# Performance work log

Hardware: AMD Instinct MI355X
Metric: run time of the kernel (lower is better)

## Reference

```python
import jax, jax.numpy as jnp
import numpy as np

EXPERT_CAPACITY = 1024  # per-batch per-expert capacity (token_priority <= capacity)


def setup_inputs() -> dict:
    key = jax.random.key(0)
    ks = jax.random.split(key, 5)
    B, S, D, FF, E = 2, 4096, 1024, 4096, 8
    return {
        "hidden_states": jax.random.normal(ks[0], (B, S, D), dtype=jnp.float32),
        "gate_w": jax.random.normal(ks[1], (D, E), dtype=jnp.float32) * (1.0 / np.sqrt(D)),
        "w1": jax.random.normal(ks[2], (E, D, FF), dtype=jnp.float32) * (1.0 / np.sqrt(D)),
        "w2": jax.random.normal(ks[3], (E, FF, D), dtype=jnp.float32) * (1.0 / np.sqrt(FF)),
        "w3": jax.random.normal(ks[4], (E, D, FF), dtype=jnp.float32) * (1.0 / np.sqrt(D)),
    }


def reference(hidden_states, gate_w, w1, w2, w3):
    B, S, D = hidden_states.shape
    E = gate_w.shape[1]
    C = EXPERT_CAPACITY

    # ---- route (jitter_noise = 0) ----
    router_logits = jnp.einsum("bsd,de->bse", hidden_states, gate_w)  # [B,S,E]
    router_probs = jax.nn.softmax(router_logits, axis=-1)
    sel = jnp.argmax(router_probs, axis=-1)  # [B,S] top-1 expert
    onehot = jax.nn.one_hot(sel, E, dtype=jnp.int32)  # [B,S,E]
    priority = jnp.cumsum(onehot, axis=1)  # cumsum over sequence (dim=-2)
    # position of token in its chosen expert's buffer (0-based)
    pos = jnp.take_along_axis(priority, sel[..., None], axis=-1)[..., 0] - 1  # [B,S]
    keep = pos < C  # token_priority <= expert_capacity
    max_prob = jnp.max(router_probs, axis=-1, keepdims=True)  # [B,S,1]

    # ---- dispatch: scatter kept tokens into [B,E,C,D]; dropped tokens have pos>=C -> mode='drop'
    b_idx = jnp.broadcast_to(jnp.arange(B)[:, None], (B, S))
    buf = jnp.zeros((B, E, C, D), dtype=hidden_states.dtype)
    buf = buf.at[b_idx, sel, pos].set(hidden_states, mode="drop")

    # ---- per-expert gated MLP (grouped GEMM): act(x@w1) * (x@w3) @ w2 ----
    g = jax.nn.silu(jnp.einsum("becd,edf->becf", buf, w1))
    u = jnp.einsum("becd,edf->becf", buf, w3)
    expert_out = jnp.einsum("becf,efd->becd", g * u, w2)  # [B,E,C,D]

    # ---- combine: kept tokens get expert output, dropped tokens keep hidden_states ----
    pos_g = jnp.minimum(pos, C - 1)  # safe gather index for dropped tokens
    gathered = expert_out[b_idx, sel, pos_g]  # [B,S,D]
    next_states = jnp.where(keep[..., None], gathered, hidden_states)
    out = max_prob * next_states  # dropout is identity (p=0)
    return out, router_logits
```

## Files before the change

### kernel.cpp

```cpp
#include <hip/hip_runtime.h>
#include <hip/hip_bf16.h>
#include <stdint.h>

#define B_  2
#define S_  4096
#define D_  1024
#define FF_ 4096
#define E_  8
#define C_  1024

typedef unsigned short u16;
typedef unsigned int   u32;
typedef float f32x4  __attribute__((ext_vector_type(4)));
typedef short bf16x8 __attribute__((ext_vector_type(8)));
typedef u16   u16x8  __attribute__((ext_vector_type(8)));

static __device__ __forceinline__ u16 f2bf(float f) {
    union { float f; u32 u; } v; v.f = f;
    u32 u = v.u;
    u32 r = (u + 0x7FFFu + ((u >> 16) & 1u)) >> 16;
    return (u16)r;
}

static __device__ __forceinline__ void gload_lds16(const u16* g, u16* l) {
    __builtin_amdgcn_global_load_lds(
        (const __attribute__((address_space(1))) u32*)g,
        (__attribute__((address_space(3))) u32*)l, 16, 0, 0);
}

#define BAR()    asm volatile("s_barrier" ::: "memory")
#define WAITV(n) asm volatile("s_waitcnt vmcnt(" #n ")" ::: "memory")
#define WAITL0() do { asm volatile("s_waitcnt lgkmcnt(0)" ::: "memory"); \
                      __builtin_amdgcn_sched_barrier(0); } while (0)

__global__ __launch_bounds__(256) void transpose_cvt(const float* __restrict__ src,
                                                     u16* __restrict__ dst, int K, int N) {
    __shared__ u16 t[64 * 64];
    size_t mat = (size_t)blockIdx.z * K * N;
    int n0 = blockIdx.x * 64, k0 = blockIdx.y * 64;
    int l = threadIdx.x & 63, w = threadIdx.x >> 6;
#pragma unroll
    for (int p = 0; p < 2; ++p) {
        int k = p * 32 + w * 8 + ((l >> 4) << 1);
        int n = (l & 15) * 4;
        float4 v0 = *(const float4*)&src[mat + (size_t)(k0 + k) * N + n0 + n];
        float4 v1 = *(const float4*)&src[mat + (size_t)(k0 + k + 1) * N + n0 + n];
        float a0[4] = {v0.x, v0.y, v0.z, v0.w};
        float a1[4] = {v1.x, v1.y, v1.z, v1.w};
#pragma unroll
        for (int j = 0; j < 4; ++j) {
            int nn = n + j;
            u32 pk = (u32)f2bf(a0[j]) | ((u32)f2bf(a1[j]) << 16);
            int slot = (k >> 3) ^ ((nn & 7) ^ ((nn >> 3) & 7));
            *(u32*)((char*)t + nn * 128 + slot * 16 + (k & 7) * 2) = pk;
        }
    }
    __syncthreads();
#pragma unroll
    for (int p = 0; p < 2; ++p) {
        int n = p * 32 + (threadIdx.x >> 3);
        int k8 = threadIdx.x & 7;
        int slot = k8 ^ ((n & 7) ^ ((n >> 3) & 7));
        u16x8 v = *(u16x8*)((char*)t + n * 128 + slot * 16);
        *(u16x8*)&dst[mat + (size_t)(n0 + n) * K + k0 + k8 * 8] = v;
    }
}

__global__ __launch_bounds__(256) void router_kernel(const float* __restrict__ hidden,
                                                     const float* __restrict__ gate_w,
                                                     float* __restrict__ logits_out,
                                                     int* __restrict__ sel,
                                                     float* __restrict__ maxp,
                                                     u16* __restrict__ xbf) {
    __shared__ float gw[D_ * E_];
    for (int i = threadIdx.x; i < D_ * E_ / 4; i += 256)
        ((float4*)gw)[i] = ((const float4*)gate_w)[i];
    __syncthreads();

    int wave = threadIdx.x >> 6, lane = threadIdx.x & 63;
    int tok = blockIdx.x * 4 + wave;
    const float* hrow = hidden + (size_t)tok * D_;
    u16* xrow = xbf + (size_t)tok * D_;

    double acc[8] = {0, 0, 0, 0, 0, 0, 0, 0};
#pragma unroll 4
    for (int i = 0; i < D_ / 64; i++) {
        int d = i * 64 + lane;
        float h = hrow[d];
        xrow[d] = f2bf(h);
        const float4* g4 = (const float4*)(gw + d * 8);
        float4 g0 = g4[0], g1 = g4[1];
        acc[0] += (double)h * g0.x; acc[1] += (double)h * g0.y;
        acc[2] += (double)h * g0.z; acc[3] += (double)h * g0.w;
        acc[4] += (double)h * g1.x; acc[5] += (double)h * g1.y;
        acc[6] += (double)h * g1.z; acc[7] += (double)h * g1.w;
    }
#pragma unroll
    for (int off = 32; off > 0; off >>= 1)
#pragma unroll
        for (int e = 0; e < 8; e++)
            acc[e] += __shfl_xor(acc[e], off);

    float l[8];
#pragma unroll
    for (int e = 0; e < 8; e++) l[e] = (float)acc[e];
    if (lane < 8) logits_out[(size_t)tok * 8 + lane] = l[lane];

    int am = 0; float mx = l[0];
#pragma unroll
    for (int e = 1; e < 8; e++) if (l[e] > mx) { mx = l[e]; am = e; }
    float sum = 0.f;
#pragma unroll
    for (int e = 0; e < 8; e++) sum += expf(l[e] - mx);
    if (lane == 0) { sel[tok] = am; maxp[tok] = 1.0f / sum; }
}

__global__ void scan_kernel(const int* __restrict__ sel, int* __restrict__ pos,
                            int* __restrict__ slot_token, int* __restrict__ counts) {
    int wave = threadIdx.x >> 6, lane = threadIdx.x & 63;
    int b = wave;
    int carry[8] = {0, 0, 0, 0, 0, 0, 0, 0};
    unsigned long long below = (lane == 0) ? 0ull : ((~0ull) >> (64 - lane));
    for (int s0 = 0; s0 < S_; s0 += 64) {
        int s = s0 + lane;
        int e = sel[b * S_ + s];
        int p = 0;
#pragma unroll
        for (int ex = 0; ex < 8; ex++) {
            unsigned long long m = __ballot(e == ex);
            if (e == ex) p = carry[ex] + (int)__popcll(m & below);
            carry[ex] += (int)__popcll(m);
        }
        pos[b * S_ + s] = p;
        if (p < C_) slot_token[(b * E_ + e) * C_ + p] = s;
    }
    if (lane < 8) {
        int c = carry[lane];
        counts[b * E_ + lane] = c < C_ ? c : C_;
    }
}

__global__ __launch_bounds__(512, 2) void gemm1_kernel(const u16* __restrict__ x,
                                                       const u16* __restrict__ w1t,
                                                       const u16* __restrict__ w3t,
                                                       const int* __restrict__ slot_token,
                                                       const int* __restrict__ counts,
                                                       u16* __restrict__ hbuf) {
    extern __shared__ u16 lds[];
    int phys = blockIdx.x + 32 * (blockIdx.y + 4 * blockIdx.z);
    int virt = (phys & 7) * 256 + (phys >> 3);
    int bx = virt & 31, by = (virt >> 5) & 3, bz = virt >> 7;

    int z = bz;
    int cnt = counts[z];
    int c0 = by * 256;
    if (c0 >= cnt) return;
    int n0 = bx * 128;
    int b = z >> 3, e = z & 7;

    int tid = threadIdx.x, w = tid >> 6, l = tid & 63;
    int wm = w >> 2, wn = w & 3;

    int arow0 = tid >> 2, arow1 = arow0 + 128;
    int lk = ((tid & 3) ^ ((tid >> 3) & 3)) * 8;
    int as0 = c0 + arow0, as1 = c0 + arow1;
    int tok0 = slot_token[z * C_ + (as0 < cnt ? as0 : 0)];
    int tok1 = slot_token[z * C_ + (as1 < cnt ? as1 : 0)];
    const u16* pA0 = x + ((size_t)(b * S_ + tok0)) * D_ + lk;
    const u16* pA1 = x + ((size_t)(b * S_ + tok1)) * D_ + lk;
    const u16* pB1 = w1t + ((size_t)e * FF_ + n0 + arow0) * D_ + lk;
    const u16* pB3 = w3t + ((size_t)e * FF_ + n0 + arow0) * D_ + lk;
    u32 wsl = (u32)w * 512;

    u32 ck  = (u32)(((l >> 4) ^ ((l >> 1) & 3)) * 8);
    u32 aoff  = (u32)(wm * 128 + (l & 15)) * 32 + ck;
    u32 b1off = 8192  + (u32)(wn * 32 + (l & 15)) * 32 + ck;
    u32 b3off = 12288 + (u32)(wn * 32 + (l & 15)) * 32 + ck;

    auto STAGE_A = [&](int t) {
        u16* Ls = lds + ((t & 3) << 14);
        int ko = t << 5;
        gload_lds16(pA0 + ko, Ls + wsl);
        gload_lds16(pA1 + ko, Ls + 4096 + wsl);
    };
    auto STAGE_B = [&](int t) {
        u16* Ls = lds + ((t & 3) << 14);
        int ko = t << 5;
        gload_lds16(pB1 + ko, Ls + 8192 + wsl);
        gload_lds16(pB3 + ko, Ls + 12288 + wsl);
    };

    f32x4 acc1[8][2] = {};
    f32x4 acc3[8][2] = {};

    constexpr int NK = D_ / 32;
    STAGE_A(0); STAGE_B(0); STAGE_A(1); STAGE_B(1); STAGE_A(2); STAGE_B(2);
    for (int t = 0; t < NK; ++t) {
        if (t + 2 < NK)      { WAITV(8); }
        else if (t + 1 < NK) { WAITV(4); }
        else                 { WAITV(0); }
        BAR();
        const u16* Ls = lds + ((t & 3) << 14);
        bf16x8 af[8], b1f[2], b3f[2];
#pragma unroll
        for (int f = 0; f < 4; f++) af[f] = *(const bf16x8*)(Ls + aoff + f * 512);
#pragma unroll
        for (int n = 0; n < 2; n++) {
            b1f[n] = *(const bf16x8*)(Ls + b1off + n * 512);
            b3f[n] = *(const bf16x8*)(Ls + b3off + n * 512);
        }
        if (t + 3 < NK) STAGE_A(t + 3);
        WAITL0();
        __builtin_amdgcn_s_setprio(1);
#pragma unroll
        for (int f = 0; f < 4; f++)
#pragma unroll
            for (int n = 0; n < 2; n++) {
                acc1[f][n] = __builtin_amdgcn_mfma_f32_16x16x32_bf16(af[f], b1f[n], acc1[f][n], 0, 0, 0);
                acc3[f][n] = __builtin_amdgcn_mfma_f32_16x16x32_bf16(af[f], b3f[n], acc3[f][n], 0, 0, 0);
            }
        __builtin_amdgcn_s_setprio(0);
        BAR();
#pragma unroll
        for (int f = 4; f < 8; f++) af[f] = *(const bf16x8*)(Ls + aoff + f * 512);
        if (t + 3 < NK) STAGE_B(t + 3);
        WAITL0();
        __builtin_amdgcn_s_setprio(1);
#pragma unroll
        for (int f = 4; f < 8; f++)
#pragma unroll
            for (int n = 0; n < 2; n++) {
                acc1[f][n] = __builtin_amdgcn_mfma_f32_16x16x32_bf16(af[f], b1f[n], acc1[f][n], 0, 0, 0);
                acc3[f][n] = __builtin_amdgcn_mfma_f32_16x16x32_bf16(af[f], b3f[n], acc3[f][n], 0, 0, 0);
            }
        __builtin_amdgcn_s_setprio(0);
    }

#pragma unroll
    for (int f = 0; f < 8; f++) {
        int row = wm * 128 + f * 16 + ((l >> 4) << 2);
#pragma unroll
        for (int r = 0; r < 4; r++) {
            int slot = c0 + row + r;
            if (slot < cnt) {
                size_t base = ((size_t)z * C_ + slot) * FF_ + n0 + wn * 32 + (l & 15);
#pragma unroll
                for (int n = 0; n < 2; n++) {
                    float g = acc1[f][n][r], uu = acc3[f][n][r];
                    float h = (g / (1.f + __expf(-g))) * uu;
                    hbuf[base + n * 16] = f2bf(h);
                }
            }
        }
    }
}

__global__ __launch_bounds__(512, 2) void gemm2_kernel(const u16* __restrict__ hbuf,
                                                       const u16* __restrict__ w2t,
                                                       const int* __restrict__ slot_token,
                                                       const int* __restrict__ counts,
                                                       const float* __restrict__ maxp,
                                                       float* __restrict__ out) {
    extern __shared__ u16 lds[];
    int phys = blockIdx.x + 4 * (blockIdx.y + 4 * blockIdx.z);
    int virt = (phys & 7) * 32 + (phys >> 3);
    int bx = virt & 3, by = (virt >> 2) & 3, bz = virt >> 4;

    int z = bz;
    int cnt = counts[z];
    int c0 = by * 256;
    if (c0 >= cnt) return;
    int n0 = bx * 256;
    int b = z >> 3, e = z & 7;

    int tid = threadIdx.x, w = tid >> 6, l = tid & 63;
    int wm = w >> 2, wn = w & 3;

    int arow0 = tid >> 2;
    int lk = ((tid & 3) ^ ((tid >> 3) & 3)) * 8;
    const u16* pA0 = hbuf + ((size_t)z * C_ + c0 + arow0) * FF_ + lk;
    const u16* pA1 = pA0 + (size_t)128 * FF_;
    const u16* pB0 = w2t + ((size_t)e * D_ + n0 + arow0) * FF_ + lk;
    const u16* pB1 = pB0 + (size_t)128 * FF_;
    u32 wsl = (u32)w * 512;

    u32 ck  = (u32)(((l >> 4) ^ ((l >> 1) & 3)) * 8);
    u32 aoff = (u32)(wm * 128 + (l & 15)) * 32 + ck;
    u32 boff = 8192 + (u32)(wn * 64 + (l & 15)) * 32 + ck;

    auto STAGE_A = [&](int t) {
        u16* Ls = lds + ((t & 3) << 14);
        int ko = t << 5;
        gload_lds16(pA0 + ko, Ls + wsl);
        gload_lds16(pA1 + ko, Ls + 4096 + wsl);
    };
    auto STAGE_B = [&](int t) {
        u16* Ls = lds + ((t & 3) << 14);
        int ko = t << 5;
        gload_lds16(pB0 + ko, Ls + 8192 + wsl);
        gload_lds16(pB1 + ko, Ls + 12288 + wsl);
    };

    f32x4 acc[8][4] = {};

    constexpr int NK = FF_ / 32;
    STAGE_A(0); STAGE_B(0); STAGE_A(1); STAGE_B(1); STAGE_A(2); STAGE_B(2);
    for (int t = 0; t < NK; ++t) {
        if (t + 2 < NK)      { WAITV(8); }
        else if (t + 1 < NK) { WAITV(4); }
        else                 { WAITV(0); }
        BAR();
        const u16* Ls = lds + ((t & 3) << 14);
        bf16x8 af[8], bfv[4];
#pragma unroll
        for (int f = 0; f < 4; f++) af[f] = *(const bf16x8*)(Ls + aoff + f * 512);
#pragma unroll
        for (int n = 0; n < 4; n++) bfv[n] = *(const bf16x8*)(Ls + boff + n * 512);
        if (t + 3 < NK) STAGE_A(t + 3);
        WAITL0();
        __builtin_amdgcn_s_setprio(1);
#pragma unroll
        for (int f = 0; f < 4; f++)
#pragma unroll
            for (int n = 0; n < 4; n++)
                acc[f][n] = __builtin_amdgcn_mfma_f32_16x16x32_bf16(af[f], bfv[n], acc[f][n], 0, 0, 0);
        __builtin_amdgcn_s_setprio(0);
        BAR();
#pragma unroll
        for (int f = 4; f < 8; f++) af[f] = *(const bf16x8*)(Ls + aoff + f * 512);
        if (t + 3 < NK) STAGE_B(t + 3);
        WAITL0();
        __builtin_amdgcn_s_setprio(1);
#pragma unroll
        for (int f = 4; f < 8; f++)
#pragma unroll
            for (int n = 0; n < 4; n++)
                acc[f][n] = __builtin_amdgcn_mfma_f32_16x16x32_bf16(af[f], bfv[n], acc[f][n], 0, 0, 0);
        __builtin_amdgcn_s_setprio(0);
    }

#pragma unroll
    for (int f = 0; f < 8; f++) {
        int row = wm * 128 + f * 16 + ((l >> 4) << 2);
#pragma unroll
        for (int r = 0; r < 4; r++) {
            int slot = c0 + row + r;
            if (slot < cnt) {
                int s = slot_token[z * C_ + slot];
                float sc = maxp[b * S_ + s];
                float* orow = out + ((size_t)b * S_ + s) * D_ + n0 + wn * 64 + (l & 15);
#pragma unroll
                for (int n = 0; n < 4; n++)
                    orow[n * 16] = sc * acc[f][n][r];
            }
        }
    }
}

__global__ __launch_bounds__(256) void combine_dropped(const float* __restrict__ hidden,
                                                       const int* __restrict__ pos,
                                                       const float* __restrict__ maxp,
                                                       float* __restrict__ out) {
    int t = blockIdx.x;
    if (pos[t] < C_) return;
    float sc = maxp[t];
    const float* src = hidden + (size_t)t * D_;
    float* dst = out + (size_t)t * D_;
    for (int d = threadIdx.x; d < D_; d += 256) dst[d] = sc * src[d];
}

extern "C" void kernel_launch(void* const* d_in, const int* in_sizes, int n_in,
                              void* d_out, int out_size, void* d_ws, size_t ws_size,
                              hipStream_t stream) {
    const float* hidden = (const float*)d_in[0];
    const float* gate_w = (const float*)d_in[1];
    const float* w1     = (const float*)d_in[2];
    const float* w2     = (const float*)d_in[3];
    const float* w3     = (const float*)d_in[4];

    float* out        = (float*)d_out;
    float* logits_out = out + (size_t)B_ * S_ * D_;

    char* ws = (char*)d_ws;
    u16* hidden_bf = (u16*)ws;            ws += (size_t)B_ * S_ * D_ * 2;
    u16* w1t       = (u16*)ws;            ws += (size_t)E_ * D_ * FF_ * 2;
    u16* w3t       = (u16*)ws;            ws += (size_t)E_ * D_ * FF_ * 2;
    u16* w2t       = (u16*)ws;            ws += (size_t)E_ * D_ * FF_ * 2;
    u16* hbuf      = (u16*)ws;            ws += (size_t)B_ * E_ * C_ * FF_ * 2;
    int*   sel        = (int*)ws;         ws += (size_t)B_ * S_ * 4;
    int*   pos        = (int*)ws;         ws += (size_t)B_ * S_ * 4;
    float* maxp       = (float*)ws;       ws += (size_t)B_ * S_ * 4;
    int*   slot_token = (int*)ws;         ws += (size_t)B_ * E_ * C_ * 4;
    int*   counts     = (int*)ws;         ws += (size_t)B_ * E_ * 4;

    (void)hipFuncSetAttribute((const void*)gemm1_kernel,
                              hipFuncAttributeMaxDynamicSharedMemorySize, 131072);
    (void)hipFuncSetAttribute((const void*)gemm2_kernel,
                              hipFuncAttributeMaxDynamicSharedMemorySize, 131072);

    router_kernel<<<B_ * S_ / 4, 256, 0, stream>>>(hidden, gate_w, logits_out, sel, maxp, hidden_bf);
    scan_kernel<<<1, 128, 0, stream>>>(sel, pos, slot_token, counts);

    transpose_cvt<<<dim3(FF_ / 64, D_ / 64, E_), 256, 0, stream>>>(w1, w1t, D_, FF_);
    transpose_cvt<<<dim3(FF_ / 64, D_ / 64, E_), 256, 0, stream>>>(w3, w3t, D_, FF_);
    transpose_cvt<<<dim3(D_ / 64, FF_ / 64, E_), 256, 0, stream>>>(w2, w2t, FF_, D_);

    gemm1_kernel<<<dim3(32, 4, 16), 512, 131072, stream>>>(hidden_bf, w1t, w3t, slot_token, counts, hbuf);
    gemm2_kernel<<<dim3(4, 4, 16), 512, 131072, stream>>>(hbuf, w2t, slot_token, counts, maxp, out);
    combine_dropped<<<B_ * S_, 256, 0, stream>>>(hidden, pos, maxp, out);
}
```

Baseline: 490.8 us.

## Pre-gather routed tokens into contiguous bf16 buffer and parallelize scan

```diff
diff --git a/kernel.cpp b/kernel.cpp
--- a/kernel.cpp
+++ b/kernel.cpp
@@ -70,8 +70,7 @@
                                                      const float* __restrict__ gate_w,
                                                      float* __restrict__ logits_out,
                                                      int* __restrict__ sel,
-                                                     float* __restrict__ maxp,
-                                                     u16* __restrict__ xbf) {
+                                                     float* __restrict__ maxp) {
     __shared__ float gw[D_ * E_];
     for (int i = threadIdx.x; i < D_ * E_ / 4; i += 256)
         ((float4*)gw)[i] = ((const float4*)gate_w)[i];
@@ -80,14 +79,12 @@
     int wave = threadIdx.x >> 6, lane = threadIdx.x & 63;
     int tok = blockIdx.x * 4 + wave;
     const float* hrow = hidden + (size_t)tok * D_;
-    u16* xrow = xbf + (size_t)tok * D_;
 
     double acc[8] = {0, 0, 0, 0, 0, 0, 0, 0};
 #pragma unroll 4
     for (int i = 0; i < D_ / 64; i++) {
         int d = i * 64 + lane;
         float h = hrow[d];
-        xrow[d] = f2bf(h);
         const float4* g4 = (const float4*)(gw + d * 8);
         float4 g0 = g4[0], g1 = g4[1];
         acc[0] += (double)h * g0.x; acc[1] += (double)h * g0.y;
@@ -115,15 +112,50 @@
     if (lane == 0) { sel[tok] = am; maxp[tok] = 1.0f / sum; }
 }
 
-__global__ void scan_kernel(const int* __restrict__ sel, int* __restrict__ pos,
-                            int* __restrict__ slot_token, int* __restrict__ counts) {
-    int wave = threadIdx.x >> 6, lane = threadIdx.x & 63;
-    int b = wave;
-    int carry[8] = {0, 0, 0, 0, 0, 0, 0, 0};
-    unsigned long long below = (lane == 0) ? 0ull : ((~0ull) >> (64 - lane));
-    for (int s0 = 0; s0 < S_; s0 += 64) {
-        int s = s0 + lane;
-        int e = sel[b * S_ + s];
+__global__ __launch_bounds__(1024) void scan_kernel(const int* __restrict__ sel,
+                                                    int* __restrict__ pos,
+                                                    int* __restrict__ slot_token,
+                                                    int* __restrict__ counts) {
+    __shared__ int hist[16][8];
+    __shared__ int base[16][8];
+    int b = blockIdx.x;
+    int tid = threadIdx.x, wv = tid >> 6, l = tid & 63;
+    unsigned long long below = (l == 0) ? 0ull : ((~0ull) >> (64 - l));
+    const int* sb = sel + b * S_;
+
+    int eloc[4];
+    int cnt[8] = {0, 0, 0, 0, 0, 0, 0, 0};
+#pragma unroll
+    for (int c = 0; c < 4; c++) {
+        int s = wv * 256 + c * 64 + l;
+        int e = sb[s];
+        eloc[c] = e;
+#pragma unroll
+        for (int ex = 0; ex < 8; ex++)
+            cnt[ex] += (int)__popcll(__ballot(e == ex));
+    }
+    if (l == 0)
+#pragma unroll
+        for (int ex = 0; ex < 8; ex++) hist[wv][ex] = cnt[ex];
+    __syncthreads();
+    if (tid < 128) {
+        int ex = tid & 7, v = tid >> 3;
+        int s = 0;
+        for (int w2 = 0; w2 < v; w2++) s += hist[w2][ex];
+        base[v][ex] = s;
+        if (v == 15) {
+            int tot = s + hist[15][ex];
+            counts[b * 8 + ex] = tot < C_ ? tot : C_;
+        }
+    }
+    __syncthreads();
+    int carry[8];
+#pragma unroll
+    for (int ex = 0; ex < 8; ex++) carry[ex] = base[wv][ex];
+#pragma unroll
+    for (int c = 0; c < 4; c++) {
+        int s = wv * 256 + c * 64 + l;
+        int e = eloc[c];
         int p = 0;
 #pragma unroll
         for (int ex = 0; ex < 8; ex++) {
@@ -134,16 +166,35 @@
         pos[b * S_ + s] = p;
         if (p < C_) slot_token[(b * E_ + e) * C_ + p] = s;
     }
-    if (lane < 8) {
-        int c = carry[lane];
-        counts[b * E_ + lane] = c < C_ ? c : C_;
-    }
-}
-
-__global__ __launch_bounds__(512, 2) void gemm1_kernel(const u16* __restrict__ x,
+}
+
+__global__ __launch_bounds__(256) void gather_kernel(const float* __restrict__ hidden,
+                                                     const int* __restrict__ slot_token,
+                                                     const int* __restrict__ counts,
+                                                     u16* __restrict__ xg) {
+    int z = blockIdx.x >> 8;
+    int r0 = (blockIdx.x & 255) * 4;
+    int cnt = counts[z];
+    int slot = r0 + (threadIdx.x >> 6);
+    if (slot >= cnt) return;
+    int l = threadIdx.x & 63;
+    int b = z >> 3;
+    int tok = slot_token[z * C_ + slot];
+    const float4* src = (const float4*)(hidden + (size_t)(b * S_ + tok) * D_) + l * 4;
+    u16x8* dst = (u16x8*)(xg + ((size_t)z * C_ + slot) * D_) + l * 2;
+#pragma unroll
+    for (int h = 0; h < 2; h++) {
+        float4 a = src[h * 2], c = src[h * 2 + 1];
+        u16x8 o;
+        o[0] = f2bf(a.x); o[1] = f2bf(a.y); o[2] = f2bf(a.z); o[3] = f2bf(a.w);
+        o[4] = f2bf(c.x); o[5] = f2bf(c.y); o[6] = f2bf(c.z); o[7] = f2bf(c.w);
+        dst[h] = o;
+    }
+}
+
+__global__ __launch_bounds__(512, 2) void gemm1_kernel(const u16* __restrict__ xg,
                                                        const u16* __restrict__ w1t,
                                                        const u16* __restrict__ w3t,
-                                                       const int* __restrict__ slot_token,
                                                        const int* __restrict__ counts,
                                                        u16* __restrict__ hbuf) {
     extern __shared__ u16 lds[];
@@ -156,21 +207,19 @@
     int c0 = by * 256;
     if (c0 >= cnt) return;
     int n0 = bx * 128;
-    int b = z >> 3, e = z & 7;
+    int e = z & 7;
 
     int tid = threadIdx.x, w = tid >> 6, l = tid & 63;
     int wm = w >> 2, wn = w & 3;
 
-    int arow0 = tid >> 2, arow1 = arow0 + 128;
+    int arow0 = tid >> 2;
     int lk = ((tid & 3) ^ ((tid >> 3) & 3)) * 8;
-    int as0 = c0 + arow0, as1 = c0 + arow1;
-    int tok0 = slot_token[z * C_ + (as0 < cnt ? as0 : 0)];
-    int tok1 = slot_token[z * C_ + (as1 < cnt ? as1 : 0)];
-    const u16* pA0 = x + ((size_t)(b * S_ + tok0)) * D_ + lk;
-    const u16* pA1 = x + ((size_t)(b * S_ + tok1)) * D_ + lk;
+    const u16* pA0 = xg + ((size_t)z * C_ + c0 + arow0) * D_ + lk;
+    const u16* pA1 = pA0 + (size_t)128 * D_;
     const u16* pB1 = w1t + ((size_t)e * FF_ + n0 + arow0) * D_ + lk;
     const u16* pB3 = w3t + ((size_t)e * FF_ + n0 + arow0) * D_ + lk;
-    u32 wsl = (u32)w * 512;
+    u32 wA0 = (u32)tid * 8, wA1 = (u32)tid * 8 + 4096;
+    u32 wB1 = 8192 + (u32)tid * 8, wB3 = 12288 + (u32)tid * 8;
 
     u32 ck  = (u32)(((l >> 4) ^ ((l >> 1) & 3)) * 8);
     u32 aoff  = (u32)(wm * 128 + (l & 15)) * 32 + ck;
@@ -180,14 +229,14 @@
     auto STAGE_A = [&](int t) {
         u16* Ls = lds + ((t & 3) << 14);
         int ko = t << 5;
-        gload_lds16(pA0 + ko, Ls + wsl);
-        gload_lds16(pA1 + ko, Ls + 4096 + wsl);
+        gload_lds16(pA0 + ko, Ls + wA0);
+        gload_lds16(pA1 + ko, Ls + wA1);
     };
     auto STAGE_B = [&](int t) {
         u16* Ls = lds + ((t & 3) << 14);
         int ko = t << 5;
-        gload_lds16(pB1 + ko, Ls + 8192 + wsl);
-        gload_lds16(pB3 + ko, Ls + 12288 + wsl);
+        gload_lds16(pB1 + ko, Ls + wB1);
+        gload_lds16(pB3 + ko, Ls + wB3);
     };
 
     f32x4 acc1[8][2] = {};
@@ -240,13 +289,13 @@
     for (int f = 0; f < 8; f++) {
         int row = wm * 128 + f * 16 + ((l >> 4) << 2);
 #pragma unroll
-        for (int r = 0; r < 4; r++) {
-            int slot = c0 + row + r;
+        for (int rr = 0; rr < 4; rr++) {
+            int slot = c0 + row + rr;
             if (slot < cnt) {
                 size_t base = ((size_t)z * C_ + slot) * FF_ + n0 + wn * 32 + (l & 15);
 #pragma unroll
                 for (int n = 0; n < 2; n++) {
-                    float g = acc1[f][n][r], uu = acc3[f][n][r];
+                    float g = acc1[f][n][rr], uu = acc3[f][n][rr];
                     float h = (g / (1.f + __expf(-g))) * uu;
                     hbuf[base + n * 16] = f2bf(h);
                 }
@@ -282,7 +331,7 @@
     const u16* pA1 = pA0 + (size_t)128 * FF_;
     const u16* pB0 = w2t + ((size_t)e * D_ + n0 + arow0) * FF_ + lk;
     const u16* pB1 = pB0 + (size_t)128 * FF_;
-    u32 wsl = (u32)w * 512;
+    u32 wsl = (u32)tid * 8;
 
     u32 ck  = (u32)(((l >> 4) ^ ((l >> 1) & 3)) * 8);
     u32 aoff = (u32)(wm * 128 + (l & 15)) * 32 + ck;
@@ -343,15 +392,15 @@
     for (int f = 0; f < 8; f++) {
         int row = wm * 128 + f * 16 + ((l >> 4) << 2);
 #pragma unroll
-        for (int r = 0; r < 4; r++) {
-            int slot = c0 + row + r;
+        for (int rr = 0; rr < 4; rr++) {
+            int slot = c0 + row + rr;
             if (slot < cnt) {
                 int s = slot_token[z * C_ + slot];
                 float sc = maxp[b * S_ + s];
                 float* orow = out + ((size_t)b * S_ + s) * D_ + n0 + wn * 64 + (l & 15);
 #pragma unroll
                 for (int n = 0; n < 4; n++)
-                    orow[n * 16] = sc * acc[f][n][r];
+                    orow[n * 16] = sc * acc[f][n][rr];
             }
         }
     }
@@ -382,7 +431,7 @@
     float* logits_out = out + (size_t)B_ * S_ * D_;
 
     char* ws = (char*)d_ws;
-    u16* hidden_bf = (u16*)ws;            ws += (size_t)B_ * S_ * D_ * 2;
+    u16* xg        = (u16*)ws;            ws += (size_t)B_ * E_ * C_ * D_ * 2;
     u16* w1t       = (u16*)ws;            ws += (size_t)E_ * D_ * FF_ * 2;
     u16* w3t       = (u16*)ws;            ws += (size_t)E_ * D_ * FF_ * 2;
     u16* w2t       = (u16*)ws;            ws += (size_t)E_ * D_ * FF_ * 2;
@@ -398,14 +447,15 @@
     (void)hipFuncSetAttribute((const void*)gemm2_kernel,
                               hipFuncAttributeMaxDynamicSharedMemorySize, 131072);
 
-    router_kernel<<<B_ * S_ / 4, 256, 0, stream>>>(hidden, gate_w, logits_out, sel, maxp, hidden_bf);
-    scan_kernel<<<1, 128, 0, stream>>>(sel, pos, slot_token, counts);
+    router_kernel<<<B_ * S_ / 4, 256, 0, stream>>>(hidden, gate_w, logits_out, sel, maxp);
+    scan_kernel<<<B_, 1024, 0, stream>>>(sel, pos, slot_token, counts);
+    gather_kernel<<<B_ * E_ * 256, 256, 0, stream>>>(hidden, slot_token, counts, xg);
 
     transpose_cvt<<<dim3(FF_ / 64, D_ / 64, E_), 256, 0, stream>>>(w1, w1t, D_, FF_);
     transpose_cvt<<<dim3(FF_ / 64, D_ / 64, E_), 256, 0, stream>>>(w3, w3t, D_, FF_);
     transpose_cvt<<<dim3(D_ / 64, FF_ / 64, E_), 256, 0, stream>>>(w2, w2t, FF_, D_);
 
-    gemm1_kernel<<<dim3(32, 4, 16), 512, 131072, stream>>>(hidden_bf, w1t, w3t, slot_token, counts, hbuf);
+    gemm1_kernel<<<dim3(32, 4, 16), 512, 131072, stream>>>(xg, w1t, w3t, counts, hbuf);
     gemm2_kernel<<<dim3(4, 4, 16), 512, 131072, stream>>>(hbuf, w2t, slot_token, counts, maxp, out);
     combine_dropped<<<B_ * S_, 256, 0, stream>>>(hidden, pos, maxp, out);
 }
```

Result: faster. 478.4 us (-2.5%).
